# Kernel tuning notes

Hardware: AMD Instinct MI355X
Metric: run time of the kernel (lower is better)

## Reference

```python
import jax, jax.numpy as jnp
import numpy as np

D_MODEL = 1024
N_HEADS = 16
D_HEAD = D_MODEL // N_HEADS
D_FF = 4096
B, T = 2, 2048


def setup_inputs() -> dict:
    key = jax.random.key(0)
    ks = jax.random.split(key, 8)
    s = 0.02
    return {
        "x": jax.random.normal(ks[0], (B, T, D_MODEL), dtype=jnp.float32),
        "wq": jax.random.normal(ks[1], (D_MODEL, D_MODEL), dtype=jnp.float32) * s,
        "wk": jax.random.normal(ks[2], (D_MODEL, D_MODEL), dtype=jnp.float32) * s,
        "wv": jax.random.normal(ks[3], (D_MODEL, D_MODEL), dtype=jnp.float32) * s,
        "wo": jax.random.normal(ks[4], (D_MODEL, D_MODEL), dtype=jnp.float32) * s,
        "w1": jax.random.normal(ks[5], (D_FF, D_MODEL), dtype=jnp.float32) * s,
        "b1": jnp.zeros((D_FF,), dtype=jnp.float32),
        "w2": jax.random.normal(ks[6], (D_MODEL, D_FF), dtype=jnp.float32) * s,
        "b2": jnp.zeros((D_MODEL,), dtype=jnp.float32),
        "ln1_g": jnp.ones((D_MODEL,), dtype=jnp.float32),
        "ln1_b": jnp.zeros((D_MODEL,), dtype=jnp.float32),
        "ln2_g": jnp.ones((D_MODEL,), dtype=jnp.float32),
        "ln2_b": jnp.zeros((D_MODEL,), dtype=jnp.float32),
    }


def _layernorm(x, g, b, eps=1e-5):
    mu = jnp.mean(x, axis=-1, keepdims=True)
    var = jnp.mean(jnp.square(x - mu), axis=-1, keepdims=True)
    return (x - mu) * jax.lax.rsqrt(var + eps) * g + b


def reference(x, wq, wk, wv, wo, w1, b1, w2, b2, ln1_g, ln1_b, ln2_g, ln2_b):
    Bsz, Tlen, C = x.shape
    h = _layernorm(x, ln1_g, ln1_b)
    # torch Linear: y = h @ W^T ; reshape to [B, H, T, Dh]
    def proj(w):
        return (h @ w.T).reshape(Bsz, Tlen, N_HEADS, D_HEAD).transpose(0, 2, 1, 3)
    q, k, v = proj(wq), proj(wk), proj(wv)
    scores = jnp.einsum('bhqd,bhkd->bhqk', q, k) / np.sqrt(D_HEAD).astype(np.float32)
    p = jax.nn.softmax(scores.astype(jnp.float32), axis=-1).astype(scores.dtype)
    out = jnp.einsum('bhqk,bhkd->bhqd', p, v)
    out = out.transpose(0, 2, 1, 3).reshape(Bsz, Tlen, C)
    x = x + out @ wo.T
    h2 = _layernorm(x, ln2_g, ln2_b)
    ff = jax.nn.gelu(h2 @ w1.T + b1, approximate=False) @ w2.T + b2
    return x + ff
```

## Files before the change

### kernel.cpp

```cpp
#include <hip/hip_runtime.h>
#include <hip/hip_bf16.h>
#include <math.h>

#define DM   1024
#define NH   16
#define DH   64
#define DFF  4096
#define BB   2
#define TT   2048
#define MTOK (BB*TT)
#define QS   3072

typedef unsigned short u16;
typedef unsigned int   u32;
typedef unsigned long long u64;
typedef __attribute__((ext_vector_type(8))) __bf16 bf16x8;
typedef __attribute__((ext_vector_type(4))) float  f32x4;

__device__ inline float bf2f(u16 u) { return __uint_as_float(((u32)u) << 16); }
__device__ inline u16 f2bf(float f) {
  u32 u = __float_as_uint(f);
  u += 0x7FFFu + ((u >> 16) & 1u);
  return (u16)(u >> 16);
}
__device__ inline u32 packtrunc(float lo, float hi) {
  return __builtin_amdgcn_perm(__float_as_uint(hi), __float_as_uint(lo), 0x07060302u);
}
__device__ inline float fexp2(float x) { return __builtin_amdgcn_exp2f(x); }

__device__ inline void gload_lds16(const void* g, void* l) {
  __builtin_amdgcn_global_load_lds(
      (const __attribute__((address_space(1))) void*)g,
      (__attribute__((address_space(3))) void*)l,
      16, 0, 0);
}

__global__ __launch_bounds__(256) void prep(
    const float* __restrict__ wq, const float* __restrict__ wk, const float* __restrict__ wv,
    const float* __restrict__ wo, const float* __restrict__ w1, const float* __restrict__ w2,
    const float* __restrict__ x, const float* __restrict__ g, const float* __restrict__ be,
    u16* __restrict__ wqkv_b, u16* __restrict__ wo_b, u16* __restrict__ w1_b,
    u16* __restrict__ w2_b, u16* __restrict__ h1)
{
  const int blk = blockIdx.x;
  if (blk < 12288) {
    const float* src; u16* dst; int idx;
    if (blk < 3072) {
      idx = blk * 256 + threadIdx.x;
      const int sel = idx >> 18;
      const int j = idx & 0x3FFFF;
      src = sel == 0 ? wq : (sel == 1 ? wk : wv);
      dst = wqkv_b;
      float4 v = ((const float4*)src)[j];
      ushort4 o; o.x = f2bf(v.x); o.y = f2bf(v.y); o.z = f2bf(v.z); o.w = f2bf(v.w);
      ((ushort4*)dst)[idx] = o;
      return;
    } else if (blk < 4096) { src = wo; dst = wo_b; idx = (blk - 3072) * 256 + threadIdx.x; }
    else if (blk < 8192)   { src = w1; dst = w1_b; idx = (blk - 4096) * 256 + threadIdx.x; }
    else                   { src = w2; dst = w2_b; idx = (blk - 8192) * 256 + threadIdx.x; }
    float4 v = ((const float4*)src)[idx];
    ushort4 o; o.x = f2bf(v.x); o.y = f2bf(v.y); o.z = f2bf(v.z); o.w = f2bf(v.w);
    ((ushort4*)dst)[idx] = o;
    return;
  }
  const int w = threadIdx.x >> 6, lane = threadIdx.x & 63;
  const int row = (blk - 12288) * 4 + w;
  const float4* xr = (const float4*)(x + (size_t)row * DM);
  float4 v[4];
  float s = 0.f, s2 = 0.f;
#pragma unroll
  for (int i = 0; i < 4; i++) {
    v[i] = xr[i * 64 + lane];
    s  += v[i].x + v[i].y + v[i].z + v[i].w;
    s2 += v[i].x * v[i].x + v[i].y * v[i].y + v[i].z * v[i].z + v[i].w * v[i].w;
  }
#pragma unroll
  for (int off = 32; off > 0; off >>= 1) {
    s  += __shfl_xor(s,  off);
    s2 += __shfl_xor(s2, off);
  }
  const float mu = s * (1.f / DM);
  const float rs = rsqrtf(s2 * (1.f / DM) - mu * mu + 1e-5f);
  u16* orow = h1 + (size_t)row * DM;
#pragma unroll
  for (int i = 0; i < 4; i++) {
    const float4 gg = ((const float4*)g)[i * 64 + lane];
    const float4 bb = ((const float4*)be)[i * 64 + lane];
    ushort4 o;
    o.x = f2bf((v[i].x - mu) * rs * gg.x + bb.x);
    o.y = f2bf((v[i].y - mu) * rs * gg.y + bb.y);
    o.z = f2bf((v[i].z - mu) * rs * gg.z + bb.z);
    o.w = f2bf((v[i].w - mu) * rs * gg.w + bb.w);
    ((ushort4*)orow)[i * 64 + lane] = o;
  }
}

__global__ __launch_bounds__(256) void ln2k(
    const float* __restrict__ xm, const float* __restrict__ g,
    const float* __restrict__ be, u16* __restrict__ h2)
{
  const int w = threadIdx.x >> 6, lane = threadIdx.x & 63;
  const int row = blockIdx.x * 4 + w;
  const size_t roff = (size_t)row * DM;
  float4 v[4];
  float s = 0.f, s2 = 0.f;
#pragma unroll
  for (int i = 0; i < 4; i++) {
    v[i] = ((const float4*)(xm + roff))[i * 64 + lane];
    s  += v[i].x + v[i].y + v[i].z + v[i].w;
    s2 += v[i].x * v[i].x + v[i].y * v[i].y + v[i].z * v[i].z + v[i].w * v[i].w;
  }
#pragma unroll
  for (int off = 32; off > 0; off >>= 1) {
    s  += __shfl_xor(s,  off);
    s2 += __shfl_xor(s2, off);
  }
  const float mu = s * (1.f / DM);
  const float rs = rsqrtf(s2 * (1.f / DM) - mu * mu + 1e-5f);
  u16* orow = h2 + roff;
#pragma unroll
  for (int i = 0; i < 4; i++) {
    const float4 gg = ((const float4*)g)[i * 64 + lane];
    const float4 bb = ((const float4*)be)[i * 64 + lane];
    ushort4 o;
    o.x = f2bf((v[i].x - mu) * rs * gg.x + bb.x);
    o.y = f2bf((v[i].y - mu) * rs * gg.y + bb.y);
    o.z = f2bf((v[i].z - mu) * rs * gg.z + bb.z);
    o.w = f2bf((v[i].w - mu) * rs * gg.w + bb.w);
    ((ushort4*)orow)[i * 64 + lane] = o;
  }
}

template <int EPI, int BN>
__global__ __launch_bounds__(256) void gemm_bt(
    const u16* __restrict__ A, const u16* __restrict__ Bw,
    int M, int N, int K,
    const float* __restrict__ bias,
    u16* __restrict__ outB, float oscale, int scaleN)
{
  constexpr int NJ = BN / 32;
  __shared__ u16 As[128 * 64];
  __shared__ u16 Bs[BN * 64];

  const int tid  = threadIdx.x;
  const int w    = tid >> 6;
  const int lane = tid & 63;
  const int wr   = w >> 1, wc = w & 1;
  const int q    = lane >> 4;
  const int li   = lane & 15;
  const int rowBase = blockIdx.y * 128;
  const int colBase = blockIdx.x * BN;

  const int lr = lane >> 3;
  const int cs = (lane & 7) ^ lr;
  const u16* Abase = A  + (size_t)(rowBase + lr) * K + cs * 8;
  const u16* Bbase = Bw + (size_t)(colBase + lr) * K + cs * 8;

  f32x4 acc[4][NJ] = {};

  for (int k0 = 0; k0 < K; k0 += 64) {
    __syncthreads();
#pragma unroll
    for (int jj = 0; jj < 4; jj++) {
      const int rb = (w * 4 + jj) * 8;
      gload_lds16(Abase + (size_t)rb * K + k0, &As[rb * 64]);
    }
#pragma unroll
    for (int jj = 0; jj < NJ; jj++) {
      const int rb = (w * NJ + jj) * 8;
      gload_lds16(Bbase + (size_t)rb * K + k0, &Bs[rb * 64]);
    }
    __syncthreads();
#pragma unroll
    for (int kk = 0; kk < 2; kk++) {
      bf16x8 fa[4], fb[NJ];
      const int pos = (kk * 4 + q) ^ (li & 7);
#pragma unroll
      for (int i = 0; i < 4; i++) {
        const int row = wr * 64 + i * 16 + li;
        fa[i] = *(const bf16x8*)&As[row * 64 + pos * 8];
      }
#pragma unroll
      for (int j = 0; j < NJ; j++) {
        const int row = wc * (BN / 2) + j * 16 + li;
        fb[j] = *(const bf16x8*)&Bs[row * 64 + pos * 8];
      }
#pragma unroll
      for (int i = 0; i < 4; i++)
#pragma unroll
        for (int j = 0; j < NJ; j++)
          acc[i][j] = __builtin_amdgcn_mfma_f32_16x16x32_bf16(fa[i], fb[j], acc[i][j], 0, 0, 0);
    }
  }

#pragma unroll
  for (int i = 0; i < 4; i++) {
#pragma unroll
    for (int j = 0; j < NJ; j++) {
      const int col = colBase + wc * (BN / 2) + j * 16 + li;
      float bv = 0.f;
      if constexpr (EPI == 2) bv = bias[col];
#pragma unroll
      for (int r = 0; r < 4; r++) {
        const int row = rowBase + wr * 64 + i * 16 + q * 4 + r;
        float v = acc[i][j][r] + bv;
        if constexpr (EPI == 2) {
          const float z = fexp2(-v * (2.302213f + 0.1029625f * v * v));
          v = v * __builtin_amdgcn_rcpf(1.f + z);
        }
        if constexpr (EPI == 0) {
          const float sc = (col < scaleN) ? oscale : 1.f;
          v *= sc;
        }
        outB[(size_t)row * N + col] = f2bf(v);
      }
    }
  }
}

template <int EPI>
__global__ __launch_bounds__(256) void gemm_f32out(
    const u16* __restrict__ A, const u16* __restrict__ Bw,
    int N, int K,
    const float* __restrict__ res, const float* __restrict__ bias,
    float* __restrict__ out)
{
  __shared__ u16 As[128 * 64];
  __shared__ u16 Bs[64 * 64];

  const int tid  = threadIdx.x;
  const int w    = tid >> 6;
  const int lane = tid & 63;
  const int wr   = w >> 1, wc = w & 1;
  const int q    = lane >> 4;
  const int li   = lane & 15;

  const int nbx = gridDim.x, nwg = nbx * gridDim.y;
  int o = blockIdx.y * nbx + blockIdx.x;
  o = (o & 7) * (nwg >> 3) + (o >> 3);
  const int rowBase = (o / nbx) * 128;
  const int colBase = (o % nbx) * 64;

  const int lr = lane >> 3;
  const int cs = (lane & 7) ^ lr;
  const u16* Abase = A  + (size_t)(rowBase + lr) * K + cs * 8;
  const u16* Bbase = Bw + (size_t)(colBase + lr) * K + cs * 8;

  f32x4 acc[4][2] = {};

  for (int k0 = 0; k0 < K; k0 += 64) {
    __syncthreads();
#pragma unroll
    for (int jj = 0; jj < 4; jj++) {
      const int rb = (w * 4 + jj) * 8;
      gload_lds16(Abase + (size_t)rb * K + k0, &As[rb * 64]);
    }
#pragma unroll
    for (int jj = 0; jj < 2; jj++) {
      const int rb = (w * 2 + jj) * 8;
      gload_lds16(Bbase + (size_t)rb * K + k0, &Bs[rb * 64]);
    }
    __syncthreads();
#pragma unroll
    for (int kk = 0; kk < 2; kk++) {
      bf16x8 fa[4], fb[2];
      const int pos = (kk * 4 + q) ^ (li & 7);
#pragma unroll
      for (int i = 0; i < 4; i++) {
        const int row = wr * 64 + i * 16 + li;
        fa[i] = *(const bf16x8*)&As[row * 64 + pos * 8];
      }
#pragma unroll
      for (int j = 0; j < 2; j++) {
        const int row = wc * 32 + j * 16 + li;
        fb[j] = *(const bf16x8*)&Bs[row * 64 + pos * 8];
      }
#pragma unroll
      for (int i = 0; i < 4; i++)
#pragma unroll
        for (int j = 0; j < 2; j++)
          acc[i][j] = __builtin_amdgcn_mfma_f32_16x16x32_bf16(fa[i], fb[j], acc[i][j], 0, 0, 0);
    }
  }

#pragma unroll
  for (int i = 0; i < 4; i++)
#pragma unroll
    for (int j = 0; j < 2; j++) {
      const int col = colBase + wc * 32 + j * 16 + li;
      float bv = 0.f;
      if constexpr (EPI == 4) bv = bias[col];
#pragma unroll
      for (int r = 0; r < 4; r++) {
        const int row = rowBase + wr * 64 + i * 16 + q * 4 + r;
        out[(size_t)row * N + col] =
            acc[i][j][r] + res[(size_t)row * N + col] + bv;
      }
    }
}

template <int EPI, int KC>
__global__ __launch_bounds__(512, 2) void gemm256(
    const u16* __restrict__ A, const u16* __restrict__ Bw,
    int N,
    const float* __restrict__ bias,
    u16* __restrict__ outB, float oscale, int scaleN)
{
  constexpr int K  = KC;
  constexpr int NT = KC / 32;
  __shared__ u16 lds[4 * 16384];

  const int tid  = threadIdx.x;
  const int w    = tid >> 6;
  const int lane = tid & 63;
  const int wr   = w >> 2, wc = w & 3;
  const int q    = lane >> 4, li = lane & 15;

  const int nbx = gridDim.x;
  const int o   = blockIdx.y * nbx + blockIdx.x;
  const int xcd = o & 7, i_x = o >> 3;
  const int nsx = nbx >> 2;
  const int super = xcd + 8 * (i_x >> 4);
  const int wi  = i_x & 15;
  const int bx  = (super % nsx) * 4 + (wi & 3);
  const int by  = (super / nsx) * 4 + (wi >> 2);
  const int rowBase = by * 256, colBase = bx * 256;

  const int srow = lane >> 2;
  const int schk = (lane & 3) ^ ((lane >> 3) & 3);
  const u16* Asrc = A  + (size_t)(rowBase + srow) * K + schk * 8;
  const u16* Bsrc = Bw + (size_t)(colBase + srow) * K + schk * 8;

  auto stageA = [&](int kt, int bsel) {
    const int k0 = kt * 32;
    u16* dst = &lds[bsel * 16384];
#pragma unroll
    for (int j = 0; j < 2; j++) {
      const int rb = w * 32 + j * 16;
      gload_lds16(Asrc + (size_t)rb * K + k0, &dst[rb * 32]);
    }
  };
  auto stageB = [&](int kt, int bsel) {
    const int k0 = kt * 32;
    u16* dst = &lds[bsel * 16384 + 8192];
#pragma unroll
    for (int j = 0; j < 2; j++) {
      const int rb = w * 32 + j * 16;
      gload_lds16(Bsrc + (size_t)rb * K + k0, &dst[rb * 32]);
    }
  };

  f32x4 acc[8][4] = {};
  const int pos = q ^ ((li >> 1) & 3);

  stageA(0, 0); stageB(0, 0);
  stageA(1, 1); stageB(1, 1);
  stageA(2, 2); stageB(2, 2);

  for (int t = 0; t < NT; ++t) {
    if (t < NT - 2)      asm volatile("s_waitcnt vmcnt(8)" ::: "memory");
    else if (t == NT - 2) asm volatile("s_waitcnt vmcnt(4)" ::: "memory");
    else                 asm volatile("s_waitcnt vmcnt(0)" ::: "memory");
    __builtin_amdgcn_s_barrier();

    const u16* bb = &lds[(t & 3) * 16384];
    bf16x8 fa[4], fb[4];

#pragma unroll
    for (int m = 0; m < 4; m++)
      fa[m] = *(const bf16x8*)&bb[(wr * 128 + m * 16 + li) * 32 + pos * 8];
#pragma unroll
    for (int n = 0; n < 4; n++)
      fb[n] = *(const bf16x8*)&bb[8192 + (wc * 64 + n * 16 + li) * 32 + pos * 8];
    if (t + 3 < NT) stageA(t + 3, (t + 3) & 3);
    __builtin_amdgcn_s_barrier();
    __builtin_amdgcn_s_setprio(1);
#pragma unroll
    for (int m = 0; m < 4; m++)
#pragma unroll
      for (int n = 0; n < 4; n++)
        acc[m][n] = __builtin_amdgcn_mfma_f32_16x16x32_bf16(fa[m], fb[n], acc[m][n], 0, 0, 0);
    __builtin_amdgcn_s_setprio(0);
    __builtin_amdgcn_s_barrier();

#pragma unroll
    for (int m = 0; m < 4; m++)
      fa[m] = *(const bf16x8*)&bb[(wr * 128 + 64 + m * 16 + li) * 32 + pos * 8];
    if (t + 3 < NT) stageB(t + 3, (t + 3) & 3);
    __builtin_amdgcn_s_barrier();
    __builtin_amdgcn_s_setprio(1);
#pragma unroll
    for (int m = 0; m < 4; m++)
#pragma unroll
      for (int n = 0; n < 4; n++)
        acc[4 + m][n] = __builtin_amdgcn_mfma_f32_16x16x32_bf16(fa[m], fb[n], acc[4 + m][n], 0, 0, 0);
    __builtin_amdgcn_s_setprio(0);
  }

#pragma unroll
  for (int n = 0; n < 4; n++) {
    const int col = colBase + wc * 64 + n * 16 + li;
    float bv = 0.f;
    if constexpr (EPI == 2) bv = bias[col];
#pragma unroll
    for (int m = 0; m < 8; m++) {
#pragma unroll
      for (int r = 0; r < 4; r++) {
        const int row = rowBase + wr * 128 + m * 16 + q * 4 + r;
        float v = acc[m][n][r] + bv;
        if constexpr (EPI == 2) {
          const float z = fexp2(-v * (2.302213f + 0.1029625f * v * v));
          v = v * __builtin_amdgcn_rcpf(1.f + z);
        }
        if constexpr (EPI == 0) {
          const float sc = (col < scaleN) ? oscale : 1.f;
          v *= sc;
        }
        outB[(size_t)row * N + col] = f2bf(v);
      }
    }
  }
}

__global__ __launch_bounds__(256) void transpose_v(
    const u16* __restrict__ vq, u16* __restrict__ vt)
{
  __shared__ u16 t[64][72];
  const int bh = blockIdx.x, b = bh >> 4, h = bh & 15;
  const int t0 = blockIdx.y * 64;
  const int tid = threadIdx.x;
  const int r = tid >> 2, c = (tid & 3) * 16;
  const u16* src = vq + (size_t)(b * TT + t0 + r) * QS + h * DH + c;
#pragma unroll
  for (int i = 0; i < 4; i++)
    *(ushort4*)&t[r][c + i * 4] = ((const ushort4*)src)[i];
  __syncthreads();
  const int dh = tid >> 2, tt = (tid & 3) * 16;
  u16* dst = vt + ((size_t)bh * 64 + dh) * TT + t0 + tt;
#pragma unroll
  for (int i = 0; i < 4; i++) {
    ushort4 o;
    o.x = t[tt + i * 4 + 0][dh]; o.y = t[tt + i * 4 + 1][dh];
    o.z = t[tt + i * 4 + 2][dh]; o.w = t[tt + i * 4 + 3][dh];
    ((ushort4*)dst)[i] = o;
  }
}

__global__ __launch_bounds__(512) void attn_mfma(
    const u16* __restrict__ qb, const u16* __restrict__ kb,
    const u16* __restrict__ vt, u16* __restrict__ ob)
{
  __shared__ u16 Ks[2][64 * 64];
  __shared__ u16 Vs[2][64 * 64];
  __shared__ u16 Sh[8 * 16 * 72];

  const int tid = threadIdx.x, w = tid >> 6, lane = tid & 63;
  const int q = lane >> 4, li = lane & 15;
  const int bh = blockIdx.x, b = bh >> 4, h = bh & 15;
  const int q0 = blockIdx.y * 128;
  const int lr8 = lane >> 3, lc8 = lane & 7;

#pragma unroll
  for (int jj = 0; jj < 2; jj++) {
    const int rb = w * 16 + jj * 8;
    const int row = rb + lr8;
    const int cs = lc8 ^ (row & 7);
    gload_lds16(qb + (size_t)(b * TT + q0 + row) * QS + h * DH + cs * 8,
                &Sh[rb * 64]);
  }
  __syncthreads();

  bf16x8 qf[2];
#pragma unroll
  for (int kk = 0; kk < 2; kk++) {
    const int row = w * 16 + li;
    const int pos = (kk * 4 + q) ^ (li & 7);
    qf[kk] = *(const bf16x8*)&Sh[row * 64 + pos * 8];
  }

  auto stage = [&](int buf, int kt) {
    const int rb = w * 8;
    const int row = rb + lr8;
    const int cs = lc8 ^ (row & 7);
    gload_lds16(kb + (size_t)(b * TT + kt + row) * QS + h * DH + cs * 8,
                &Ks[buf][rb * 64]);
    gload_lds16(vt + ((size_t)bh * 64 + row) * TT + kt + cs * 8,
                &Vs[buf][rb * 64]);
  };

  f32x4 ot[4] = {};
  float lsum = 0.f;
  u16* Pw = &Sh[w * 16 * 72];

  stage(0, 0);
  for (int it = 0; it < TT / 64; it++) {
    __syncthreads();
    if (it + 1 < TT / 64) stage((it + 1) & 1, (it + 1) * 64);
    const u16* Kc = Ks[it & 1];
    const u16* Vc = Vs[it & 1];

    f32x4 st[4] = {};
#pragma unroll
    for (int kk = 0; kk < 2; kk++)
#pragma unroll
      for (int i = 0; i < 4; i++) {
        const int pos = (kk * 4 + q) ^ (li & 7);
        const bf16x8 kf = *(const bf16x8*)&Kc[(i * 16 + li) * 64 + pos * 8];
        st[i] = __builtin_amdgcn_mfma_f32_16x16x32_bf16(kf, qf[kk], st[i], 0, 0, 0);
      }

    u64 pk[4];
#pragma unroll
    for (int i = 0; i < 4; i++) {
      const float p0 = fexp2(st[i][0]);
      const float p1 = fexp2(st[i][1]);
      const float p2 = fexp2(st[i][2]);
      const float p3 = fexp2(st[i][3]);
      lsum += (p0 + p1) + (p2 + p3);
      pk[i] = ((u64)packtrunc(p2, p3) << 32) | packtrunc(p0, p1);
    }

#pragma unroll
    for (int i = 0; i < 4; i++)
      *(u64*)&Pw[li * 72 + i * 16 + q * 4] = pk[i];

#pragma unroll
    for (int kk = 0; kk < 2; kk++) {
      const bf16x8 pf = *(const bf16x8*)&Pw[li * 72 + kk * 32 + q * 8];
#pragma unroll
      for (int m = 0; m < 4; m++) {
        const int pos = (kk * 4 + q) ^ (li & 7);
        const bf16x8 vf = *(const bf16x8*)&Vc[(m * 16 + li) * 64 + pos * 8];
        ot[m] = __builtin_amdgcn_mfma_f32_16x16x32_bf16(vf, pf, ot[m], 0, 0, 0);
      }
    }
  }

  float s = lsum;
  s += __shfl_xor(s, 16);
  s += __shfl_xor(s, 32);
  const float inv = 1.f / s;
#pragma unroll
  for (int m = 0; m < 4; m++) {
    const u64 pv = ((u64)packtrunc(ot[m][2] * inv, ot[m][3] * inv) << 32)
                 | packtrunc(ot[m][0] * inv, ot[m][1] * inv);
    *(u64*)&Pw[li * 72 + m * 16 + q * 4] = pv;
  }
#pragma unroll
  for (int pass = 0; pass < 2; pass++) {
    const int row = pass * 8 + lr8;
    const bf16x8 v = *(const bf16x8*)&Pw[row * 72 + lc8 * 8];
    const int token = q0 + w * 16 + row;
    *(bf16x8*)(ob + ((size_t)(b * TT + token) * NH + h) * DH + lc8 * 8) = v;
  }
}

extern "C" void kernel_launch(void* const* d_in, const int* in_sizes, int n_in,
                              void* d_out, int out_size, void* d_ws, size_t ws_size,
                              hipStream_t stream) {
  const float* x    = (const float*)d_in[0];
  const float* wq   = (const float*)d_in[1];
  const float* wk   = (const float*)d_in[2];
  const float* wv   = (const float*)d_in[3];
  const float* wo   = (const float*)d_in[4];
  const float* w1   = (const float*)d_in[5];
  const float* b1   = (const float*)d_in[6];
  const float* w2   = (const float*)d_in[7];
  const float* b2   = (const float*)d_in[8];
  const float* ln1g = (const float*)d_in[9];
  const float* ln1b = (const float*)d_in[10];
  const float* ln2g = (const float*)d_in[11];
  const float* ln2b = (const float*)d_in[12];

  size_t off = 0;
  char* base = (char*)d_ws;
  auto alloc = [&](size_t bytes) { void* p = base + off; off += bytes; return p; };

  u16* wqkv_b = (u16*)alloc((size_t)3 * DM * DM * 2);
  u16* wo_b   = (u16*)alloc((size_t)DM * DM * 2);
  u16* w1_b   = (u16*)alloc((size_t)DFF * DM * 2);
  u16* w2_b   = (u16*)alloc((size_t)DM * DFF * 2);
  u16* h1     = (u16*)alloc((size_t)MTOK * DM * 2);
  u16* qkvb   = (u16*)alloc((size_t)MTOK * QS * 2);
  u16* attn   = (u16*)alloc((size_t)MTOK * DM * 2);
  u16* h2     = (u16*)alloc((size_t)MTOK * DM * 2);
  u16* ff1    = (u16*)alloc((size_t)MTOK * DFF * 2);
  float* xmid = (float*)alloc((size_t)MTOK * DM * 4);
  u16* vtb    = ff1;
  (void)ws_size; (void)in_sizes; (void)n_in; (void)out_size;

  prep<<<13312, 256, 0, stream>>>(wq, wk, wv, wo, w1, w2, x, ln1g, ln1b,
                                  wqkv_b, wo_b, w1_b, w2_b, h1);

  const float QSCALE = 0.125f * 1.44269504088896340736f;
  gemm_bt<0, 128><<<dim3(QS / 128, MTOK / 128), 256, 0, stream>>>(
      h1, wqkv_b, MTOK, QS, DM, nullptr, qkvb, QSCALE, DM);

  transpose_v<<<dim3(BB * NH, TT / 64), 256, 0, stream>>>(qkvb + 2 * DM, vtb);
  attn_mfma<<<dim3(BB * NH, TT / 128), 512, 0, stream>>>(qkvb, qkvb + DM, vtb, attn);

  gemm_f32out<3><<<dim3(DM / 64, MTOK / 128), 256, 0, stream>>>(
      attn, wo_b, DM, DM, x, nullptr, xmid);
  ln2k<<<MTOK / 4, 256, 0, stream>>>(xmid, ln2g, ln2b, h2);

  gemm256<2, DM><<<dim3(DFF / 256, MTOK / 256), 512, 0, stream>>>(
      h2, w1_b, DFF, b1, ff1, 1.f, 0);
  gemm_f32out<4><<<dim3(DM / 64, MTOK / 128), 256, 0, stream>>>(
      ff1, w2_b, DM, DFF, xmid, b2, (float*)d_out);
}
```

Before: 330.3 us.

## Split-K the FF2 GEMM with a separate reduction and swizzle GEMM block order

The final FF2 GEMM (K=4096) is split into two K-halves that write fp32 partial tiles into the dead h1/qkv workspace. A new elementwise kernel then sums both partials with the residual and b2 to produce the output. This is meant to raise parallelism and shorten the long K loop per block. A block-index swizzle is also added to the QKV GEMM and the new kernel to improve L2 locality. In exchange it writes and reads large fp32 partial buffers and adds one kernel launch.

```diff
diff --git a/kernel.cpp b/kernel.cpp
--- a/kernel.cpp
+++ b/kernel.cpp
@@ -131,6 +131,23 @@
   }
 }
 
+__global__ __launch_bounds__(256) void reduce_out(
+    const float* __restrict__ Q, const float* __restrict__ xmid,
+    const float* __restrict__ b2, float* __restrict__ out)
+{
+  const float* Q0 = Q;
+  const float* Q1 = Q + (size_t)MTOK * DM;
+  const int i = blockIdx.x * 256 + threadIdx.x;
+  const float4 a = ((const float4*)xmid)[i];
+  const float4 p = ((const float4*)Q0)[i];
+  const float4 qv = ((const float4*)Q1)[i];
+  const float4 bb = ((const float4*)b2)[i & (DM / 4 - 1)];
+  float4 o;
+  o.x = a.x + p.x + qv.x + bb.x; o.y = a.y + p.y + qv.y + bb.y;
+  o.z = a.z + p.z + qv.z + bb.z; o.w = a.w + p.w + qv.w + bb.w;
+  ((float4*)out)[i] = o;
+}
+
 template <int EPI, int BN>
 __global__ __launch_bounds__(256) void gemm_bt(
     const u16* __restrict__ A, const u16* __restrict__ Bw,
@@ -148,8 +165,12 @@
   const int wr   = w >> 1, wc = w & 1;
   const int q    = lane >> 4;
   const int li   = lane & 15;
-  const int rowBase = blockIdx.y * 128;
-  const int colBase = blockIdx.x * BN;
+
+  const int nbx = gridDim.x, nwg = nbx * gridDim.y;
+  int o = blockIdx.y * nbx + blockIdx.x;
+  o = (o & 7) * (nwg >> 3) + (o >> 3);
+  const int rowBase = (o / nbx) * 128;
+  const int colBase = (o % nbx) * BN;
 
   const int lr = lane >> 3;
   const int cs = (lane & 7) ^ lr;
@@ -420,6 +441,83 @@
       }
     }
   }
+}
+
+__global__ __launch_bounds__(256) void gemm_sk(
+    const u16* __restrict__ A, const u16* __restrict__ Bw,
+    int N, int K, int KLEN, float* __restrict__ P)
+{
+  __shared__ u16 As[128 * 64];
+  __shared__ u16 Bs[64 * 64];
+
+  const int tid  = threadIdx.x;
+  const int w    = tid >> 6;
+  const int lane = tid & 63;
+  const int wr   = w >> 1, wc = w & 1;
+  const int q    = lane >> 4;
+  const int li   = lane & 15;
+
+  const int nbx = gridDim.x, nwg = nbx * gridDim.y;
+  int o = blockIdx.y * nbx + blockIdx.x;
+  o = (o & 7) * (nwg >> 3) + (o >> 3);
+  const int rowBase = (o / nbx) * 128;
+  const int colBase = (o % nbx) * 64;
+  const int koff = blockIdx.z * KLEN;
+
+  const int lr = lane >> 3;
+  const int cs = (lane & 7) ^ lr;
+  const u16* Abase = A  + (size_t)(rowBase + lr) * K + koff + cs * 8;
+  const u16* Bbase = Bw + (size_t)(colBase + lr) * K + koff + cs * 8;
+
+  f32x4 acc[4][2] = {};
+
+  for (int k0 = 0; k0 < KLEN; k0 += 64) {
+    __syncthreads();
+#pragma unroll
+    for (int jj = 0; jj < 4; jj++) {
+      const int rb = (w * 4 + jj) * 8;
+      gload_lds16(Abase + (size_t)rb * K + k0, &As[rb * 64]);
+    }
+#pragma unroll
+    for (int jj = 0; jj < 2; jj++) {
+      const int rb = (w * 2 + jj) * 8;
+      gload_lds16(Bbase + (size_t)rb * K + k0, &Bs[rb * 64]);
+    }
+    __syncthreads();
+#pragma unroll
+    for (int kk = 0; kk < 2; kk++) {
+      bf16x8 fa[4], fb[2];
+      const int pos = (kk * 4 + q) ^ (li & 7);
+#pragma unroll
+      for (int i = 0; i < 4; i++) {
+        const int row = wr * 64 + i * 16 + li;
+        fa[i] = *(const bf16x8*)&As[row * 64 + pos * 8];
+      }
+#pragma unroll
+      for (int j = 0; j < 2; j++) {
+        const int row = wc * 32 + j * 16 + li;
+        fb[j] = *(const bf16x8*)&Bs[row * 64 + pos * 8];
+      }
+#pragma unroll
+      for (int i = 0; i < 4; i++)
+#pragma unroll
+        for (int j = 0; j < 2; j++)
+          acc[i][j] = __builtin_amdgcn_mfma_f32_16x16x32_bf16(fa[i], fb[j], acc[i][j], 0, 0, 0);
+    }
+  }
+
+  float* Pz = P + (size_t)blockIdx.z * MTOK * DM;
+#pragma unroll
+  for (int i = 0; i < 4; i++)
+#pragma unroll
+    for (int j = 0; j < 2; j++) {
+      const int col = colBase + wc * 32 + j * 16 + li;
+#pragma unroll
+      for (int r = 0; r < 4; r++) {
+        const int row = rowBase + wr * 64 + i * 16 + q * 4 + r;
+        Pz[(size_t)row * N + col] = acc[i][j][r];
+      }
+    }
 }
 
 __global__ __launch_bounds__(256) void transpose_v(
@@ -587,6 +685,7 @@
   u16* ff1    = (u16*)alloc((size_t)MTOK * DFF * 2);
   float* xmid = (float*)alloc((size_t)MTOK * DM * 4);
   u16* vtb    = ff1;
+  float* ff2P = (float*)h1;
   (void)ws_size; (void)in_sizes; (void)n_in; (void)out_size;
 
   prep<<<13312, 256, 0, stream>>>(wq, wk, wv, wo, w1, w2, x, ln1g, ln1b,
@@ -605,6 +704,7 @@
 
   gemm256<2, DM><<<dim3(DFF / 256, MTOK / 256), 512, 0, stream>>>(
       h2, w1_b, DFF, b1, ff1, 1.f, 0);
-  gemm_f32out<4><<<dim3(DM / 64, MTOK / 128), 256, 0, stream>>>(
-      ff1, w2_b, DM, DFF, xmid, b2, (float*)d_out);
-}
+  gemm_sk<<<dim3(DM / 64, MTOK / 128, 2), 256, 0, stream>>>(
+      ff1, w2_b, DM, DFF, DFF / 2, ff2P);
+  reduce_out<<<MTOK * DM / 4 / 256, 256, 0, stream>>>(ff2P, xmid, b2, (float*)d_out);
+}
```

Measured after the change: 326.0 us. No clear change (-1.3%).
